# Kernel tuning notes

Measured on AMD Instinct MI355X. Metric: run time of the kernel, lower is better.

The kernel has to match this reference:

```python
import jax, jax.numpy as jnp
import numpy as np

N = 100000      # nodes in batch / feature table
S = 25          # sampled neighbors per node (nsamples)
F_IN = 128      # in_features
F_OUT = 128     # out_features


def setup_inputs() -> dict:
    key = jax.random.key(0)
    k1, k2, k3, k4 = jax.random.split(key, 4)
    x = jax.random.normal(k1, (N, F_IN), dtype=jnp.float32)
    neighbor_idx = jax.random.randint(k2, (N, S), 0, N, dtype=jnp.int64)
    stdv = 1.0 / np.sqrt(F_OUT)
    W = jax.random.uniform(k3, (F_IN, F_OUT), dtype=jnp.float32, minval=-stdv, maxval=stdv)
    b = jax.random.uniform(k4, (F_OUT,), dtype=jnp.float32, minval=-stdv, maxval=stdv)
    return {"x": x, "neighbor_idx": neighbor_idx, "W": W, "b": b}


def reference(x, neighbor_idx, W, b):
    # GraphSage-style mean aggregator: gather sampled neighbor features
    # [N, S, F_IN], average together with the self feature, then project.
    neigh = jnp.take(x, neighbor_idx, axis=0)          # [N, S, F_IN] (irregular gather)
    agg = (x + neigh.sum(axis=1)) / jnp.float32(S + 1)  # mean over {self} U neighbors
    return agg @ W + b                                  # [N, F_OUT]
```

## Files before the change

kernel.cpp:

```cpp
#include <hip/hip_runtime.h>

#define F 128
#define S 25

typedef __attribute__((ext_vector_type(8))) short bf16x8;
typedef __attribute__((ext_vector_type(4))) float f32x4;

__device__ __forceinline__ ushort f2bf(float f) {
    uint u = __float_as_uint(f);
    return (ushort)((u + 0x7FFFu + ((u >> 16) & 1u)) >> 16);
}
__device__ __forceinline__ float bf_lo(uint v) { return __uint_as_float(v << 16); }
__device__ __forceinline__ float bf_hi(uint v) { return __uint_as_float(v & 0xFFFF0000u); }

__device__ __forceinline__ bool idx_is_i64(const int* __restrict__ p) {
    return (p[1] | p[3] | p[5] | p[7]) == 0;
}
__device__ __forceinline__ int load_idx(const int* __restrict__ p, size_t i, bool is64) {
    return is64 ? p[2 * i] : p[i];
}

__global__ __launch_bounds__(256) void gemm_xw_bf16(
    const float* __restrict__ x, const float* __restrict__ W,
    ushort* __restrict__ y, int N)
{
    __shared__ ushort WF[4][8][64][8];

    const int tid  = threadIdx.x;
    const int lane = tid & 63;
    const int wid  = tid >> 6;

    for (int e = tid; e < 4 * 8 * 64; e += 256) {
        const int l  = e & 63;
        const int nt = (e >> 6) & 7;
        const int kt = e >> 9;
        const int k0 = kt * 32 + (l >> 4) * 8;
        const int n  = nt * 16 + (l & 15);
        #pragma unroll
        for (int b = 0; b < 8; ++b)
            WF[kt][nt][l][b] = f2bf(W[(size_t)(k0 + b) * F + n]);
    }
    __syncthreads();

    const int n0 = blockIdx.x * 64 + wid * 16;
    const int arow = n0 + (lane & 15);
    const int arow_c = arow < N ? arow : N - 1;
    const float* xrow = x + (size_t)arow_c * F + (lane >> 4) * 8;

    f32x4 acc[8];
    #pragma unroll
    for (int nt = 0; nt < 8; ++nt) acc[nt] = (f32x4){0.f, 0.f, 0.f, 0.f};

    #pragma unroll
    for (int kt = 0; kt < 4; ++kt) {
        float4 a0 = *(const float4*)(xrow + kt * 32);
        float4 a1 = *(const float4*)(xrow + kt * 32 + 4);
        bf16x8 af;
        af[0] = (short)f2bf(a0.x); af[1] = (short)f2bf(a0.y);
        af[2] = (short)f2bf(a0.z); af[3] = (short)f2bf(a0.w);
        af[4] = (short)f2bf(a1.x); af[5] = (short)f2bf(a1.y);
        af[6] = (short)f2bf(a1.z); af[7] = (short)f2bf(a1.w);
        #pragma unroll
        for (int nt = 0; nt < 8; ++nt) {
            bf16x8 bf = *(const bf16x8*)&WF[kt][nt][lane][0];
            acc[nt] = __builtin_amdgcn_mfma_f32_16x16x32_bf16(af, bf, acc[nt], 0, 0, 0);
        }
    }

    const int drow0 = n0 + (lane >> 4) * 4;
    const int dcol  = lane & 15;
    #pragma unroll
    for (int nt = 0; nt < 8; ++nt) {
        #pragma unroll
        for (int r = 0; r < 4; ++r) {
            const int row = drow0 + r;
            if (row < N)
                y[(size_t)row * F + nt * 16 + dcol] = f2bf(acc[nt][r]);
        }
    }
}

__global__ __launch_bounds__(256) void gather_agg_bf16(
    const ushort* __restrict__ y, const int* __restrict__ nbr,
    const float* __restrict__ bias, float* __restrict__ out, int N)
{
    const int lane = threadIdx.x & 63;
    const int wid  = threadIdx.x >> 6;
    const bool is64 = idx_is_i64(nbr);
    const float2 bb = ((const float2*)bias)[lane];
    const float inv = 1.0f / (float)(S + 1);
    const int nw = gridDim.x * 4;
    const uint* yw = (const uint*)y;

    for (int n = blockIdx.x * 4 + wid; n < N; n += nw) {
        const int nu = __builtin_amdgcn_readfirstlane(n);

        int ids[S];
        #pragma unroll
        for (int s = 0; s < S; ++s)
            ids[s] = load_idx(nbr, (size_t)nu * S + s, is64);

        uint vs[S];
        #pragma unroll
        for (int s = 0; s < S; ++s)
            vs[s] = yw[(size_t)ids[s] * 64 + lane];
        const uint v0 = yw[(size_t)nu * 64 + lane];

        float ax = bf_lo(v0), ay = bf_hi(v0);
        #pragma unroll
        for (int s = 0; s < S; ++s) {
            ax += bf_lo(vs[s]);
            ay += bf_hi(vs[s]);
        }
        float2 o;
        o.x = ax * inv + bb.x;
        o.y = ay * inv + bb.y;
        ((float2*)(out + (size_t)nu * F))[lane] = o;
    }
}

__global__ __launch_bounds__(256) void fused_fallback_kernel(
    const float* __restrict__ x, const int* __restrict__ nbr,
    const float* __restrict__ W, const float* __restrict__ bias,
    float* __restrict__ out, int N)
{
    __shared__ float aggs[4][F];
    const int lane = threadIdx.x & 63;
    const int wid  = threadIdx.x >> 6;
    const bool is64 = idx_is_i64(nbr);
    const float inv = 1.0f / (float)(S + 1);
    const int stride = gridDim.x * 4;

    for (int base = blockIdx.x * 4; base < N; base += stride) {
        int n = base + wid;
        bool act = n < N;
        float2 acc = make_float2(0.f, 0.f);
        if (act) {
            acc = ((const float2*)(x + (size_t)n * F))[lane];
            for (int s = 0; s < S; ++s) {
                int id = load_idx(nbr, (size_t)n * S + s, is64);
                float2 v = ((const float2*)(x + (size_t)id * F))[lane];
                acc.x += v.x; acc.y += v.y;
            }
        }
        aggs[wid][2 * lane]     = acc.x * inv;
        aggs[wid][2 * lane + 1] = acc.y * inv;
        __syncthreads();
        if (act) {
            float o0 = bias[lane], o1 = bias[lane + 64];
            for (int k = 0; k < F; ++k) {
                float a = aggs[wid][k];
                o0 += a * W[k * F + lane];
                o1 += a * W[k * F + lane + 64];
            }
            out[(size_t)n * F + lane]      = o0;
            out[(size_t)n * F + lane + 64] = o1;
        }
        __syncthreads();
    }
}

extern "C" void kernel_launch(void* const* d_in, const int* in_sizes, int n_in,
                              void* d_out, int out_size, void* d_ws, size_t ws_size,
                              hipStream_t stream) {
    const float* x    = (const float*)d_in[0];
    const int*   nbr  = (const int*)d_in[1];
    const float* W    = (const float*)d_in[2];
    const float* bias = (const float*)d_in[3];
    float* out = (float*)d_out;
    const int N = in_sizes[0] / F;
    const size_t need = (size_t)N * F * sizeof(ushort);

    if (ws_size >= need) {
        ushort* y = (ushort*)d_ws;
        const int tiles = (N + 63) / 64;
        gemm_xw_bf16<<<tiles, 256, 0, stream>>>(x, W, y, N);
        gather_agg_bf16<<<2048, 256, 0, stream>>>(y, nbr, bias, out, N);
    } else {
        fused_fallback_kernel<<<2048, 256, 0, stream>>>(x, nbr, W, bias, out, N);
    }
}
```

Before: 127.7 us.

## Chunk projected features by column block and gather per chunk with compacted indices

The GEMM now writes its bf16 output in a chunked layout of 8 column blocks of 16 features, so each chunk of the table is contiguous (N x 32 bytes). A new gather kernel assigns one block per (64-node tile, chunk), stages the neighbor indices in LDS, and reads 4-byte pieces from a much smaller per-chunk working set. The intent is better L2/MALL locality for the random gathers. It adds an index-compaction pre-pass that narrows int64 indices to int32, which costs an extra kernel launch and extra memory traffic, and the indices are reread once per chunk.

```diff
diff --git a/kernel.cpp b/kernel.cpp
--- a/kernel.cpp
+++ b/kernel.cpp
@@ -2,9 +2,12 @@
 
 #define F 128
 #define S 25
+#define CH 8
+#define CW 16
 
 typedef __attribute__((ext_vector_type(8))) short bf16x8;
 typedef __attribute__((ext_vector_type(4))) float f32x4;
+typedef __attribute__((ext_vector_type(2))) float f32x2;
 
 __device__ __forceinline__ ushort f2bf(float f) {
     uint u = __float_as_uint(f);
@@ -20,6 +23,15 @@
     return is64 ? p[2 * i] : p[i];
 }
 
+__global__ __launch_bounds__(256) void compact_idx(
+    const int* __restrict__ src, int* __restrict__ dst, int M)
+{
+    const bool is64 = idx_is_i64(src);
+    int e = blockIdx.x * 256 + threadIdx.x;
+    if (e < M) dst[e] = load_idx(src, (size_t)e, is64);
+}
+
+template <int CHUNKED>
 __global__ __launch_bounds__(256) void gemm_xw_bf16(
     const float* __restrict__ x, const float* __restrict__ W,
     ushort* __restrict__ y, int N)
@@ -74,8 +86,63 @@
         #pragma unroll
         for (int r = 0; r < 4; ++r) {
             const int row = drow0 + r;
-            if (row < N)
-                y[(size_t)row * F + nt * 16 + dcol] = f2bf(acc[nt][r]);
+            if (row < N) {
+                if (CHUNKED)
+                    y[((size_t)nt * N + row) * CW + dcol] = f2bf(acc[nt][r]);
+                else
+                    y[(size_t)row * F + nt * 16 + dcol] = f2bf(acc[nt][r]);
+            }
+        }
+    }
+}
+
+__global__ __launch_bounds__(256) void gather_chunked(
+    const ushort* __restrict__ y, const int* __restrict__ idx32,
+    const float* __restrict__ bias, float* __restrict__ out, int N)
+{
+    __shared__ int IDX[64 * S];
+
+    const int tid   = threadIdx.x;
+    const int chunk = blockIdx.x & 7;
+    const int tile  = blockIdx.x >> 3;
+    const int nbase = tile * 64;
+    const long total = (long)N * S;
+
+    for (int e = tid; e < 64 * S; e += 256) {
+        long p = (long)nbase * S + e;
+        IDX[e] = (p < total) ? __builtin_nontemporal_load(&idx32[p]) : 0;
+    }
+    __syncthreads();
+
+    const int lane = tid & 63, wave = tid >> 6;
+    const int g = lane >> 3, j = lane & 7;
+    const float2 bb = *(const float2*)(bias + chunk * CW + 2 * j);
+    const float inv = 1.0f / (float)(S + 1);
+    const char* ycb = (const char*)(y + (size_t)chunk * N * CW);
+
+    #pragma unroll
+    for (int oct = 0; oct < 2; ++oct) {
+        const int nl = wave * 16 + oct * 8 + g;
+        const int n  = nbase + nl;
+        const int nc = n < N ? n : 0;
+
+        uint v[26];
+        v[25] = *(const uint*)(ycb + (((uint)nc) << 5) + (j << 2));
+        #pragma unroll
+        for (int s = 0; s < S; ++s) {
+            int id = IDX[nl * S + s];
+            v[s] = *(const uint*)(ycb + (((uint)id) << 5) + (j << 2));
+        }
+
+        float ax = 0.f, ay = 0.f;
+        #pragma unroll
+        for (int s = 0; s < 26; ++s) { ax += bf_lo(v[s]); ay += bf_hi(v[s]); }
+
+        if (n < N) {
+            f32x2 o;
+            o.x = ax * inv + bb.x;
+            o.y = ay * inv + bb.y;
+            __builtin_nontemporal_store(o, (f32x2*)(out + (size_t)n * F + chunk * CW + 2 * j));
         }
     }
 }
@@ -94,24 +161,18 @@
 
     for (int n = blockIdx.x * 4 + wid; n < N; n += nw) {
         const int nu = __builtin_amdgcn_readfirstlane(n);
-
         int ids[S];
         #pragma unroll
         for (int s = 0; s < S; ++s)
             ids[s] = load_idx(nbr, (size_t)nu * S + s, is64);
-
         uint vs[S];
         #pragma unroll
         for (int s = 0; s < S; ++s)
             vs[s] = yw[(size_t)ids[s] * 64 + lane];
         const uint v0 = yw[(size_t)nu * 64 + lane];
-
         float ax = bf_lo(v0), ay = bf_hi(v0);
         #pragma unroll
-        for (int s = 0; s < S; ++s) {
-            ax += bf_lo(vs[s]);
-            ay += bf_hi(vs[s]);
-        }
+        for (int s = 0; s < S; ++s) { ax += bf_lo(vs[s]); ay += bf_hi(vs[s]); }
         float2 o;
         o.x = ax * inv + bb.x;
         o.y = ay * inv + bb.y;
@@ -169,12 +230,21 @@
     const float* bias = (const float*)d_in[3];
     float* out = (float*)d_out;
     const int N = in_sizes[0] / F;
-    const size_t need = (size_t)N * F * sizeof(ushort);
-
-    if (ws_size >= need) {
+    const int M = N * S;
+
+    const size_t y_bytes   = (size_t)N * F * sizeof(ushort);
+    const size_t idx_bytes = (size_t)M * sizeof(int);
+
+    if (ws_size >= y_bytes + idx_bytes) {
+        ushort* y   = (ushort*)d_ws;
+        int*  idx32 = (int*)((char*)d_ws + y_bytes);
+        compact_idx<<<(M + 255) / 256, 256, 0, stream>>>(nbr, idx32, M);
+        gemm_xw_bf16<1><<<(N + 63) / 64, 256, 0, stream>>>(x, W, y, N);
+        const int tiles = (N + 63) / 64;
+        gather_chunked<<<tiles * CH, 256, 0, stream>>>(y, idx32, bias, out, N);
+    } else if (ws_size >= y_bytes) {
         ushort* y = (ushort*)d_ws;
-        const int tiles = (N + 63) / 64;
-        gemm_xw_bf16<<<tiles, 256, 0, stream>>>(x, W, y, N);
+        gemm_xw_bf16<0><<<(N + 63) / 64, 256, 0, stream>>>(x, W, y, N);
         gather_agg_bf16<<<2048, 256, 0, stream>>>(y, nbr, bias, out, N);
     } else {
         fused_fallback_kernel<<<2048, 256, 0, stream>>>(x, nbr, W, bias, out, N);
```

Result: slower. 145.9 us (+14.3%).
